# Performance work log

Hardware: AMD Instinct MI355X
Metric: run time of the kernel (lower is better)

## Reference

```python
import jax, jax.numpy as jnp
import numpy as np

B, N, DEG = 128, 512, 8          # graphs, nodes per graph, avg degree
E = B * N * DEG                  # 524288 edges
F_IN, H1, H2, C = 128, 64, 128, 10
RATIO = 0.8
K = int(np.ceil(RATIO * N))      # TopKPooling keeps ceil(0.8*N)=410 nodes per graph


def setup_inputs() -> dict:
    key = jax.random.key(0)
    ks = jax.random.split(key, 10)
    n_nodes = B * N
    x = jax.random.normal(ks[0], (n_nodes, F_IN), dtype=jnp.float32)
    # random intra-graph edges, then offset node ids per graph
    src = jax.random.randint(ks[1], (B, N * DEG), 0, N)
    dst = jax.random.randint(ks[2], (B, N * DEG), 0, N)
    off = (jnp.arange(B) * N)[:, None]
    edge_index = jnp.stack([(src + off).reshape(-1), (dst + off).reshape(-1)]).astype(jnp.int64)
    batch = jnp.repeat(jnp.arange(B), N).astype(jnp.int64)
    s1 = 1.0 / np.sqrt(F_IN)
    s2 = 1.0 / np.sqrt(H1)
    s3 = 1.0 / np.sqrt(H2)
    return {
        "x": x,
        "edge_index": edge_index,
        "batch": batch,
        "W1": jax.random.uniform(ks[3], (F_IN, H1), jnp.float32, -s1, s1),
        "b1": jnp.zeros((H1,), jnp.float32),
        "W2": jax.random.uniform(ks[4], (H1, H2), jnp.float32, -s2, s2),
        "b2": jnp.zeros((H2,), jnp.float32),
        "pool_w": jax.random.uniform(ks[5], (H2,), jnp.float32, -s3, s3),
        "fc_W": jax.random.uniform(ks[6], (H2, C), jnp.float32, -s3, s3),
        "fc_b": jax.random.uniform(ks[7], (C,), jnp.float32, -s3, s3),
    }


def gcn_conv(x, W, b, src, dst, num_nodes):
    # PyG GCNConv: add self-loops, symmetric normalization, scatter-add aggregation
    loop = jnp.arange(num_nodes)
    src = jnp.concatenate([src, loop])
    dst = jnp.concatenate([dst, loop])
    deg = jax.ops.segment_sum(jnp.ones_like(src, dtype=x.dtype), dst, num_segments=num_nodes)
    dis = jnp.where(deg > 0, jax.lax.rsqrt(jnp.maximum(deg, 1.0)), 0.0)
    norm = dis[src] * dis[dst]                       # [E+N]
    h = x @ W                                        # transform first (smaller of the two in conv1)
    out = jax.ops.segment_sum(norm[:, None] * h[src], dst, num_segments=num_nodes)
    return out + b


def reference(x, edge_index, batch, W1, b1, W2, b2, pool_w, fc_W, fc_b):
    num_nodes = x.shape[0]
    src, dst = edge_index[0], edge_index[1]
    x = jax.nn.relu(gcn_conv(x, W1, b1, src, dst, num_nodes))
    x = jax.nn.relu(gcn_conv(x, W2, b2, src, dst, num_nodes))
    # TopKPooling: score = (x . w)/||w||, per-graph top-k on raw score, gate by tanh(score)
    score = (x @ pool_w) / jnp.linalg.norm(pool_w)   # [B*N]
    score_b = score.reshape(B, N)
    top_vals, top_idx = jax.lax.top_k(score_b, K)    # [B, K]
    x_b = x.reshape(B, N, H2)
    x_sel = jnp.take_along_axis(x_b, top_idx[:, :, None], axis=1)   # [B, K, H2]
    x_sel = x_sel * jnp.tanh(top_vals)[:, :, None]
    # global max pool over each (pooled) graph; pooled edge_index is unused downstream
    g = jnp.max(x_sel, axis=1)                        # [B, H2]
    logits = g @ fc_W + fc_b                          # [B, C]
    return jax.nn.log_softmax(logits, axis=1)
```

## Files before the change

kernel.cpp:

```cpp
#include <hip/hip_runtime.h>
#include <hip/hip_bf16.h>


#define BB 128
#define NN 512
#define NODES (BB*NN)
#define EE (BB*NN*8)
#define EDGPG (NN*8)
#define F_IN 128
#define H1 64
#define H2 128
#define NC 10
#define KSEL 410
#define ROWCAP 48

typedef unsigned short u16;
typedef unsigned int   u32;

static __device__ __forceinline__ float lo2f(u32 u){ return __uint_as_float(u << 16); }
static __device__ __forceinline__ float hi2f(u32 u){ return __uint_as_float(u & 0xffff0000u); }
static __device__ __forceinline__ u16 f2b(float f){
    __hip_bfloat16 h = __float2bfloat16(f);
    return *reinterpret_cast<u16*>(&h);
}
static __device__ __forceinline__ u32 packbf(float a, float b){
    return (u32)f2b(a) | ((u32)f2b(b) << 16);
}
static __device__ __forceinline__ void acc8s(float* a, uint4 v, float ds){
    a[0] = fmaf(ds, lo2f(v.x), a[0]); a[1] = fmaf(ds, hi2f(v.x), a[1]);
    a[2] = fmaf(ds, lo2f(v.y), a[2]); a[3] = fmaf(ds, hi2f(v.y), a[3]);
    a[4] = fmaf(ds, lo2f(v.z), a[4]); a[5] = fmaf(ds, hi2f(v.z), a[5]);
    a[6] = fmaf(ds, lo2f(v.w), a[6]); a[7] = fmaf(ds, hi2f(v.w), a[7]);
}
static __device__ __forceinline__ void acc8(float* a, uint4 v){
    a[0] += lo2f(v.x); a[1] += hi2f(v.x);
    a[2] += lo2f(v.y); a[3] += hi2f(v.y);
    a[4] += lo2f(v.z); a[5] += hi2f(v.z);
    a[6] += lo2f(v.w); a[7] += hi2f(v.w);
}
static __device__ __forceinline__ int swz2048(int bid){
    return ((bid & 7) << 8) | (bid >> 3);
}
static __device__ __forceinline__ int swz1024(int bid){
    return ((bid & 7) << 7) | (bid >> 3);
}

static __device__ __forceinline__ bool ei_is_i64(const int* __restrict__ ei){
    return ((ei[1] | ei[3] | ei[5] | ei[7]) == 0);
}
static __device__ __forceinline__ int ld_src(const int* __restrict__ ei, int e, bool w64){
    return w64 ? ei[2*e] : ei[e];
}
static __device__ __forceinline__ int ld_dst(const int* __restrict__ ei, int e, bool w64){
    return w64 ? ei[2*(EE + e)] : ei[EE + e];
}

__global__ __launch_bounds__(512) void k_build(const int* __restrict__ ei,
                                               int* __restrict__ cnt,
                                               int* __restrict__ adj){
    bool w64 = ei_is_i64(ei);
    int t = threadIdx.x;
    int e = (int)blockIdx.x*512 + t;
    int b = e >> 12;
    int d = (ld_dst(ei, e, w64) - b*NN) & (NN - 1);
    int s = ld_src(ei, e, w64) & (NODES - 1);
    int node = b*NN + d;
    int p = atomicAdd(&cnt[node], 1);
    if (p < ROWCAP - 1) adj[node*ROWCAP + 1 + p] = s;
    if (blockIdx.x < BB){
        int sn = (int)blockIdx.x*NN + t;
        adj[sn*ROWCAP] = sn;
    }
}

#define G1NODES 64
#define XPAD 68
__global__ __launch_bounds__(512) void k_gemm1(const float* __restrict__ x,
                                               const float* __restrict__ W1,
                                               u32* __restrict__ h1u){
    __shared__ __align__(16) float Ws[64*H1];
    __shared__ __align__(16) float xs[G1NODES*XPAD];
    int t = threadIdx.x;
    int node0 = (int)blockIdx.x*G1NODES;
    int tc = t & 15, tr = t >> 4;
    int j0 = tc*4, n0 = tr*2;
    float acc[2][4] = {};
    for (int half = 0; half < 2; ++half){
        const float4* Wv = (const float4*)(W1 + half*4096);
        for (int i = t; i < 1024; i += 512)
            *(float4*)&Ws[i*4] = Wv[i];
        for (int i = t; i < 1024; i += 512){
            int node = i >> 4, c = i & 15;
            float4 v = *(const float4*)(x + (size_t)(node0 + node)*F_IN + half*64 + c*4);
            *(float4*)&xs[node*XPAD + c*4] = v;
        }
        __syncthreads();
        #pragma unroll 2
        for (int k = 0; k < 64; k += 4){
            float4 xv0 = *(const float4*)&xs[(n0+0)*XPAD + k];
            float4 xv1 = *(const float4*)&xs[(n0+1)*XPAD + k];
            float xa0[4] = {xv0.x, xv0.y, xv0.z, xv0.w};
            float xa1[4] = {xv1.x, xv1.y, xv1.z, xv1.w};
            #pragma unroll
            for (int kk = 0; kk < 4; ++kk){
                float4 wv = *(const float4*)&Ws[(k+kk)*H1 + j0];
                acc[0][0] += xa0[kk]*wv.x; acc[0][1] += xa0[kk]*wv.y; acc[0][2] += xa0[kk]*wv.z; acc[0][3] += xa0[kk]*wv.w;
                acc[1][0] += xa1[kk]*wv.x; acc[1][1] += xa1[kk]*wv.y; acc[1][2] += xa1[kk]*wv.z; acc[1][3] += xa1[kk]*wv.w;
            }
        }
        __syncthreads();
    }
    #pragma unroll
    for (int i = 0; i < 2; ++i){
        int node = node0 + n0 + i;
        size_t base = (size_t)node*32 + tc*2;
        h1u[base]     = packbf(acc[i][0], acc[i][1]);
        h1u[base + 1] = packbf(acc[i][2], acc[i][3]);
    }
}

__global__ __launch_bounds__(256) void k_agg1(const uint4* __restrict__ h1v,
                                              const int* __restrict__ cnt,
                                              const int* __restrict__ adj,
                                              const float4* __restrict__ b1v,
                                              uint4* __restrict__ a1v){
    __shared__ float disl[NN];
    int t = threadIdx.x;
    int lb = swz2048((int)blockIdx.x);
    int node0 = lb*32;
    int gbase = node0 & ~(NN - 1);
    for (int i = t; i < NN; i += 256){
        int c = cnt[gbase + i]; if (c > ROWCAP-1) c = ROWCAP-1;
        disl[i] = rsqrtf((float)(c + 1));
    }
    __syncthreads();
    int node = node0 + (t >> 3);
    int fl = t & 7;
    int rs = node*ROWCAP;
    int c = cnt[node]; if (c > ROWCAP-1) c = ROWCAP-1;
    int pe = rs + c + 1;
    float a0[8] = {}, a1r[8] = {}, a2r[8] = {}, a3r[8] = {};
    int p = rs;
    for (; p + 4 <= pe; p += 4){
        int s0 = adj[p], s1 = adj[p+1], s2 = adj[p+2], s3 = adj[p+3];
        float d0 = disl[s0 & (NN-1)], d1 = disl[s1 & (NN-1)];
        float d2 = disl[s2 & (NN-1)], d3 = disl[s3 & (NN-1)];
        uint4 v0 = h1v[s0*8 + fl];
        uint4 v1 = h1v[s1*8 + fl];
        uint4 v2 = h1v[s2*8 + fl];
        uint4 v3 = h1v[s3*8 + fl];
        acc8s(a0, v0, d0); acc8s(a1r, v1, d1); acc8s(a2r, v2, d2); acc8s(a3r, v3, d3);
    }
    for (; p < pe; ++p){
        int s = adj[p];
        acc8s(a0, h1v[s*8 + fl], disl[s & (NN-1)]);
    }
    float r[8];
    #pragma unroll
    for (int j = 0; j < 8; ++j) r[j] = (a0[j] + a1r[j]) + (a2r[j] + a3r[j]);
    float dn = disl[node & (NN-1)];
    float4 bA = b1v[2*fl], bB = b1v[2*fl+1];
    float w0 = dn*r[0] + bA.x; w0 = w0 > 0.f ? w0 : 0.f;
    float w1 = dn*r[1] + bA.y; w1 = w1 > 0.f ? w1 : 0.f;
    float w2 = dn*r[2] + bA.z; w2 = w2 > 0.f ? w2 : 0.f;
    float w3 = dn*r[3] + bA.w; w3 = w3 > 0.f ? w3 : 0.f;
    float w4 = dn*r[4] + bB.x; w4 = w4 > 0.f ? w4 : 0.f;
    float w5 = dn*r[5] + bB.y; w5 = w5 > 0.f ? w5 : 0.f;
    float w6 = dn*r[6] + bB.z; w6 = w6 > 0.f ? w6 : 0.f;
    float w7 = dn*r[7] + bB.w; w7 = w7 > 0.f ? w7 : 0.f;
    a1v[node*8 + fl] = make_uint4(packbf(dn*w0, dn*w1), packbf(dn*w2, dn*w3),
                                  packbf(dn*w4, dn*w5), packbf(dn*w6, dn*w7));
}

#define G2NODES 64
#define APAD 68
__global__ __launch_bounds__(256) void k_gemm2s(const uint4* __restrict__ a1v,
                                                const int* __restrict__ cnt,
                                                const int* __restrict__ adj,
                                                const float* __restrict__ W2,
                                                const float* __restrict__ b2,
                                                const float* __restrict__ pw,
                                                u32* __restrict__ a2u,
                                                float* __restrict__ score){
    __shared__ __align__(16) float Ws[32*H2];
    __shared__ __align__(16) float as[G2NODES*APAD];
    __shared__ float pws[H2];
    int t = threadIdx.x;
    int lb = swz1024((int)blockIdx.x);
    int node0 = lb*G2NODES;
    if (t < H2) pws[t] = pw[t];
    {
        int fl = t & 7, ng = t >> 3;
        for (int pass = 0; pass < 2; ++pass){
            int nl = ng + pass*32;
            int node = node0 + nl;
            int rs = node*ROWCAP;
            int c = cnt[node]; if (c > ROWCAP-1) c = ROWCAP-1;
            int pe = rs + c + 1;
            float a0[8] = {}, a1r[8] = {}, a2r[8] = {}, a3r[8] = {};
            int p = rs;
            for (; p + 4 <= pe; p += 4){
                int s0 = adj[p], s1 = adj[p+1], s2 = adj[p+2], s3 = adj[p+3];
                uint4 v0 = a1v[s0*8 + fl];
                uint4 v1 = a1v[s1*8 + fl];
                uint4 v2 = a1v[s2*8 + fl];
                uint4 v3 = a1v[s3*8 + fl];
                acc8(a0, v0); acc8(a1r, v1); acc8(a2r, v2); acc8(a3r, v3);
            }
            for (; p < pe; ++p){
                uint4 v = a1v[adj[p]*8 + fl];
                acc8(a0, v);
            }
            float dn = rsqrtf((float)(c + 1));
            float* dst = &as[nl*APAD + 8*fl];
            float r0 = dn*((a0[0] + a1r[0]) + (a2r[0] + a3r[0]));
            float r1 = dn*((a0[1] + a1r[1]) + (a2r[1] + a3r[1]));
            float r2 = dn*((a0[2] + a1r[2]) + (a2r[2] + a3r[2]));
            float r3 = dn*((a0[3] + a1r[3]) + (a2r[3] + a3r[3]));
            float r4 = dn*((a0[4] + a1r[4]) + (a2r[4] + a3r[4]));
            float r5 = dn*((a0[5] + a1r[5]) + (a2r[5] + a3r[5]));
            float r6 = dn*((a0[6] + a1r[6]) + (a2r[6] + a3r[6]));
            float r7 = dn*((a0[7] + a1r[7]) + (a2r[7] + a3r[7]));
            *(float4*)&dst[0] = make_float4(r0, r1, r2, r3);
            *(float4*)&dst[4] = make_float4(r4, r5, r6, r7);
        }
    }
    int tc = t & 15, tr = t >> 4;
    int j0 = tc*8;
    float acc[4][8] = {};
    for (int half = 0; half < 2; ++half){
        const float4* Wv = (const float4*)(W2 + half*4096);
        for (int i = t; i < 1024; i += 256)
            *(float4*)&Ws[i*4] = Wv[i];
        __syncthreads();
        int kb = half*32;
        #pragma unroll 2
        for (int k = 0; k < 32; k += 4){
            float4 xv0 = *(const float4*)&as[(tr +  0)*APAD + kb + k];
            float4 xv1 = *(const float4*)&as[(tr + 16)*APAD + kb + k];
            float4 xv2 = *(const float4*)&as[(tr + 32)*APAD + kb + k];
            float4 xv3 = *(const float4*)&as[(tr + 48)*APAD + kb + k];
            float xa0[4] = {xv0.x, xv0.y, xv0.z, xv0.w};
            float xa1[4] = {xv1.x, xv1.y, xv1.z, xv1.w};
            float xa2[4] = {xv2.x, xv2.y, xv2.z, xv2.w};
            float xa3[4] = {xv3.x, xv3.y, xv3.z, xv3.w};
            #pragma unroll
            for (int kk = 0; kk < 4; ++kk){
                float4 wa = *(const float4*)&Ws[(k+kk)*H2 + j0];
                float4 wb = *(const float4*)&Ws[(k+kk)*H2 + j0 + 4];
                acc[0][0] += xa0[kk]*wa.x; acc[0][1] += xa0[kk]*wa.y; acc[0][2] += xa0[kk]*wa.z; acc[0][3] += xa0[kk]*wa.w;
                acc[0][4] += xa0[kk]*wb.x; acc[0][5] += xa0[kk]*wb.y; acc[0][6] += xa0[kk]*wb.z; acc[0][7] += xa0[kk]*wb.w;
                acc[1][0] += xa1[kk]*wa.x; acc[1][1] += xa1[kk]*wa.y; acc[1][2] += xa1[kk]*wa.z; acc[1][3] += xa1[kk]*wa.w;
                acc[1][4] += xa1[kk]*wb.x; acc[1][5] += xa1[kk]*wb.y; acc[1][6] += xa1[kk]*wb.z; acc[1][7] += xa1[kk]*wb.w;
                acc[2][0] += xa2[kk]*wa.x; acc[2][1] += xa2[kk]*wa.y; acc[2][2] += xa2[kk]*wa.z; acc[2][3] += xa2[kk]*wa.w;
                acc[2][4] += xa2[kk]*wb.x; acc[2][5] += xa2[kk]*wb.y; acc[2][6] += xa2[kk]*wb.z; acc[2][7] += xa2[kk]*wb.w;
                acc[3][0] += xa3[kk]*wa.x; acc[3][1] += xa3[kk]*wa.y; acc[3][2] += xa3[kk]*wa.z; acc[3][3] += xa3[kk]*wa.w;
                acc[3][4] += xa3[kk]*wb.x; acc[3][5] += xa3[kk]*wb.y; acc[3][6] += xa3[kk]*wb.z; acc[3][7] += xa3[kk]*wb.w;
            }
        }
        __syncthreads();
    }
    float p0 = pws[j0],   p1 = pws[j0+1], p2 = pws[j0+2], p3 = pws[j0+3];
    float p4 = pws[j0+4], p5 = pws[j0+5], p6 = pws[j0+6], p7 = pws[j0+7];
    float bj[8];
    #pragma unroll
    for (int c2 = 0; c2 < 8; ++c2) bj[c2] = b2[j0 + c2];
    #pragma unroll
    for (int i = 0; i < 4; ++i){
        int node = node0 + tr + 16*i;
        float v0 = acc[i][0] + bj[0]; v0 = v0 > 0.f ? v0 : 0.f;
        float v1 = acc[i][1] + bj[1]; v1 = v1 > 0.f ? v1 : 0.f;
        float v2 = acc[i][2] + bj[2]; v2 = v2 > 0.f ? v2 : 0.f;
        float v3 = acc[i][3] + bj[3]; v3 = v3 > 0.f ? v3 : 0.f;
        float v4 = acc[i][4] + bj[4]; v4 = v4 > 0.f ? v4 : 0.f;
        float v5 = acc[i][5] + bj[5]; v5 = v5 > 0.f ? v5 : 0.f;
        float v6 = acc[i][6] + bj[6]; v6 = v6 > 0.f ? v6 : 0.f;
        float v7 = acc[i][7] + bj[7]; v7 = v7 > 0.f ? v7 : 0.f;
        *(uint4*)&a2u[(size_t)node*64 + tc*4] =
            make_uint4(packbf(v0, v1), packbf(v2, v3), packbf(v4, v5), packbf(v6, v7));
        float sp = v0*p0 + v1*p1 + v2*p2 + v3*p3 + v4*p4 + v5*p5 + v6*p6 + v7*p7;
        sp += __shfl_xor(sp, 8, 16);
        sp += __shfl_xor(sp, 4, 16);
        sp += __shfl_xor(sp, 2, 16);
        sp += __shfl_xor(sp, 1, 16);
        if (tc == 0) score[node] = sp;
    }
}

__global__ __launch_bounds__(512) void k_pool(const u32* __restrict__ a2u,
                                              const float* __restrict__ score,
                                              const float* __restrict__ pw,
                                              const float* __restrict__ fcW,
                                              const float* __restrict__ fcb,
                                              float* __restrict__ out){
    __shared__ float so[NN];
    __shared__ float ss[NN];
    __shared__ float th[NN];
    __shared__ float pm[32*H2];
    __shared__ float gl[H2];
    __shared__ float fws[H2*NC];
    __shared__ float lg[NC];
    __shared__ float red[3];
    int b = blockIdx.x, t = threadIdx.x;
    for (int i = t; i < H2*NC; i += 512) fws[i] = fcW[i];
    if (t < H2){ float v = pw[t]; gl[t] = v*v; }
    __syncthreads();
    if (t == 0){
        float s = 0.f;
        for (int i = 0; i < H2; ++i) s += gl[i];
        red[2] = rsqrtf(s);
    }
    __syncthreads();
    float pwinv = red[2];
    float sc = score[b*NN + t];
    so[t] = sc; th[t] = tanhf(sc*pwinv);
    float v = sc;
    for (int k = 2; k <= NN; k <<= 1){
        for (int j = k >> 1; j > 0; j >>= 1){
            bool desc  = ((t & k) == 0);
            bool lower = ((t & j) == 0);
            bool wantmax = (desc == lower);
            float c;
            if (j >= 64){
                ss[t] = v; __syncthreads();
                c = ss[t ^ j];
                __syncthreads();
            } else {
                c = __shfl_xor(v, j, 64);
            }
            v = wantmax ? fmaxf(v, c) : fminf(v, c);
        }
    }
    ss[t] = v;
    __syncthreads();
    float thresh = ss[KSEL-1];
    float mask_t = (so[t] >= thresh) ? 0.f : -INFINITY;
    __syncthreads();
    so[t] = mask_t;
    __syncthreads();
    int tc = t & 15, q = t >> 4;
    const uint4* ap = (const uint4*)(a2u + (size_t)b*NN*64);
    float m0 = -INFINITY, m1 = -INFINITY, m2 = -INFINITY, m3 = -INFINITY;
    float m4 = -INFINITY, m5 = -INFINITY, m6 = -INFINITY, m7 = -INFINITY;
    int nb = q*16;
    #pragma unroll 4
    for (int n = nb; n < nb + 16; ++n){
        uint4 vv = ap[(size_t)n*16 + tc];
        float thn = th[n], son = so[n];
        m0 = fmaxf(m0, lo2f(vv.x)*thn + son);
        m1 = fmaxf(m1, hi2f(vv.x)*thn + son);
        m2 = fmaxf(m2, lo2f(vv.y)*thn + son);
        m3 = fmaxf(m3, hi2f(vv.y)*thn + son);
        m4 = fmaxf(m4, lo2f(vv.z)*thn + son);
        m5 = fmaxf(m5, hi2f(vv.z)*thn + son);
        m6 = fmaxf(m6, lo2f(vv.w)*thn + son);
        m7 = fmaxf(m7, hi2f(vv.w)*thn + son);
    }
    float* pmr = &pm[q*H2 + 8*tc];
    pmr[0] = m0; pmr[1] = m1; pmr[2] = m2; pmr[3] = m3;
    pmr[4] = m4; pmr[5] = m5; pmr[6] = m6; pmr[7] = m7;
    __syncthreads();
    if (t < H2){
        float g = pm[t];
        #pragma unroll
        for (int qq = 1; qq < 32; ++qq) g = fmaxf(g, pm[qq*H2 + t]);
        gl[t] = g;
    }
    __syncthreads();
    if (t < NC){
        float acc = fcb[t];
        for (int k2 = 0; k2 < H2; ++k2) acc += gl[k2]*fws[k2*NC + t];
        lg[t] = acc;
    }
    __syncthreads();
    if (t == 0){
        float mx = lg[0];
        for (int i = 1; i < NC; ++i) mx = fmaxf(mx, lg[i]);
        float s = 0.f;
        for (int i = 0; i < NC; ++i) s += expf(lg[i] - mx);
        red[0] = mx; red[1] = logf(s);
    }
    __syncthreads();
    if (t < NC) out[b*NC + t] = lg[t] - red[0] - red[1];
}

extern "C" void kernel_launch(void* const* d_in, const int* in_sizes, int n_in,
                              void* d_out, int out_size, void* d_ws, size_t ws_size,
                              hipStream_t stream) {
    const float* x   = (const float*)d_in[0];
    const int*   ei  = (const int*)d_in[1];
    const float* W1  = (const float*)d_in[3];
    const float* b1  = (const float*)d_in[4];
    const float* W2  = (const float*)d_in[5];
    const float* b2  = (const float*)d_in[6];
    const float* pw  = (const float*)d_in[7];
    const float* fcW = (const float*)d_in[8];
    const float* fcb = (const float*)d_in[9];

    char* ws = (char*)d_ws;
    int*   cnt   = (int*)(ws + 4096);
    float* score = (float*)(ws + 524288);
    int*   adj   = (int*)(ws + 4194304);
    u32*   h1u   = (u32*)(ws + 16777216);
    u32*   a1u   = (u32*)(ws + 25165824);
    u32*   a2u   = (u32*)(ws + 33554432);

    hipMemsetAsync(cnt, 0, NODES*sizeof(int), stream);
    k_build<<<EE/512, 512, 0, stream>>>(ei, cnt, adj);
    k_gemm1<<<NODES/G1NODES, 512, 0, stream>>>(x, W1, h1u);
    k_agg1<<<NODES/32, 256, 0, stream>>>((const uint4*)h1u, cnt, adj,
                                         (const float4*)b1, (uint4*)a1u);
    k_gemm2s<<<NODES/G2NODES, 256, 0, stream>>>((const uint4*)a1u, cnt, adj,
                                                W2, b2, pw, a2u, score);
    k_pool<<<BB, 512, 0, stream>>>(a2u, score, pw, fcW, fcb, (float*)d_out);
}
```

Measured before the change: 181.5 us.

## Fuse adjacency build into gemm1, split layer-2 aggregation from its GEMM

Measured after the change: 180.9 us. No clear change (-0.3%).

```diff
diff --git a/kernel.cpp b/kernel.cpp
--- a/kernel.cpp
+++ b/kernel.cpp
@@ -55,33 +55,36 @@
     return w64 ? ei[2*(EE + e)] : ei[EE + e];
 }
 
-__global__ __launch_bounds__(512) void k_build(const int* __restrict__ ei,
-                                               int* __restrict__ cnt,
-                                               int* __restrict__ adj){
+#define G1NODES 64
+#define XPAD 68
+__global__ __launch_bounds__(512) void k_prep_gemm1(const int* __restrict__ ei,
+                                                    const float* __restrict__ x,
+                                                    const float* __restrict__ W1,
+                                                    int* __restrict__ cnt,
+                                                    int* __restrict__ adj,
+                                                    u32* __restrict__ h1u){
+    __shared__ __align__(16) float Ws[64*H1];
+    __shared__ __align__(16) float xs[G1NODES*XPAD];
     bool w64 = ei_is_i64(ei);
     int t = threadIdx.x;
-    int e = (int)blockIdx.x*512 + t;
-    int b = e >> 12;
-    int d = (ld_dst(ei, e, w64) - b*NN) & (NN - 1);
-    int s = ld_src(ei, e, w64) & (NODES - 1);
-    int node = b*NN + d;
-    int p = atomicAdd(&cnt[node], 1);
-    if (p < ROWCAP - 1) adj[node*ROWCAP + 1 + p] = s;
-    if (blockIdx.x < BB){
-        int sn = (int)blockIdx.x*NN + t;
-        adj[sn*ROWCAP] = sn;
-    }
-}
-
-#define G1NODES 64
-#define XPAD 68
-__global__ __launch_bounds__(512) void k_gemm1(const float* __restrict__ x,
-                                               const float* __restrict__ W1,
-                                               u32* __restrict__ h1u){
-    __shared__ __align__(16) float Ws[64*H1];
-    __shared__ __align__(16) float xs[G1NODES*XPAD];
-    int t = threadIdx.x;
-    int node0 = (int)blockIdx.x*G1NODES;
+    int gb = (int)blockIdx.x;
+    int b  = gb >> 3;
+    int sub = gb & 7;
+    int node0 = b*NN + sub*G1NODES;
+
+    {
+        int e = b*EDGPG + sub*512 + t;
+        int d = (ld_dst(ei, e, w64) - b*NN) & (NN - 1);
+        int s = ld_src(ei, e, w64) & (NODES - 1);
+        int node = b*NN + d;
+        int p = atomicAdd(&cnt[node], 1);
+        if (p < ROWCAP - 1) adj[node*ROWCAP + 1 + p] = s;
+    }
+    if (t < G1NODES){
+        int node = node0 + t;
+        adj[node*ROWCAP] = node;
+    }
+
     int tc = t & 15, tr = t >> 4;
     int j0 = tc*4, n0 = tr*2;
     float acc[2][4] = {};
@@ -172,16 +175,49 @@
                                   packbf(dn*w4, dn*w5), packbf(dn*w6, dn*w7));
 }
 
+__global__ __launch_bounds__(256) void k_agg2(const uint4* __restrict__ a1v,
+                                              const int* __restrict__ cnt,
+                                              const int* __restrict__ adj,
+                                              float4* __restrict__ aggf){
+    int t = threadIdx.x;
+    int lb = swz2048((int)blockIdx.x);
+    int node = lb*32 + (t >> 3);
+    int fl = t & 7;
+    int rs = node*ROWCAP;
+    int c = cnt[node]; if (c > ROWCAP-1) c = ROWCAP-1;
+    int pe = rs + c + 1;
+    float a0[8] = {}, b0[8] = {}, c0[8] = {}, d0[8] = {};
+    int p = rs;
+    for (; p + 4 <= pe; p += 4){
+        int s0 = adj[p], s1 = adj[p+1], s2 = adj[p+2], s3 = adj[p+3];
+        uint4 v0 = a1v[s0*8 + fl];
+        uint4 v1 = a1v[s1*8 + fl];
+        uint4 v2 = a1v[s2*8 + fl];
+        uint4 v3 = a1v[s3*8 + fl];
+        acc8(a0, v0); acc8(b0, v1); acc8(c0, v2); acc8(d0, v3);
+    }
+    for (; p < pe; ++p) acc8(a0, a1v[adj[p]*8 + fl]);
+    float dn = rsqrtf((float)(c + 1));
+    float r0 = dn*((a0[0]+b0[0]) + (c0[0]+d0[0]));
+    float r1 = dn*((a0[1]+b0[1]) + (c0[1]+d0[1]));
+    float r2 = dn*((a0[2]+b0[2]) + (c0[2]+d0[2]));
+    float r3 = dn*((a0[3]+b0[3]) + (c0[3]+d0[3]));
+    float r4 = dn*((a0[4]+b0[4]) + (c0[4]+d0[4]));
+    float r5 = dn*((a0[5]+b0[5]) + (c0[5]+d0[5]));
+    float r6 = dn*((a0[6]+b0[6]) + (c0[6]+d0[6]));
+    float r7 = dn*((a0[7]+b0[7]) + (c0[7]+d0[7]));
+    aggf[(size_t)node*16 + fl*2]     = make_float4(r0, r1, r2, r3);
+    aggf[(size_t)node*16 + fl*2 + 1] = make_float4(r4, r5, r6, r7);
+}
+
 #define G2NODES 64
 #define APAD 68
-__global__ __launch_bounds__(256) void k_gemm2s(const uint4* __restrict__ a1v,
-                                                const int* __restrict__ cnt,
-                                                const int* __restrict__ adj,
-                                                const float* __restrict__ W2,
-                                                const float* __restrict__ b2,
-                                                const float* __restrict__ pw,
-                                                u32* __restrict__ a2u,
-                                                float* __restrict__ score){
+__global__ __launch_bounds__(512) void k_gemm2sc(const float4* __restrict__ aggf,
+                                                 const float* __restrict__ W2,
+                                                 const float* __restrict__ b2,
+                                                 const float* __restrict__ pw,
+                                                 u32* __restrict__ a2u,
+                                                 float* __restrict__ score){
     __shared__ __align__(16) float Ws[32*H2];
     __shared__ __align__(16) float as[G2NODES*APAD];
     __shared__ float pws[H2];
@@ -189,73 +225,39 @@
     int lb = swz1024((int)blockIdx.x);
     int node0 = lb*G2NODES;
     if (t < H2) pws[t] = pw[t];
-    {
-        int fl = t & 7, ng = t >> 3;
-        for (int pass = 0; pass < 2; ++pass){
-            int nl = ng + pass*32;
-            int node = node0 + nl;
-            int rs = node*ROWCAP;
-            int c = cnt[node]; if (c > ROWCAP-1) c = ROWCAP-1;
-            int pe = rs + c + 1;
-            float a0[8] = {}, a1r[8] = {}, a2r[8] = {}, a3r[8] = {};
-            int p = rs;
-            for (; p + 4 <= pe; p += 4){
-                int s0 = adj[p], s1 = adj[p+1], s2 = adj[p+2], s3 = adj[p+3];
-                uint4 v0 = a1v[s0*8 + fl];
-                uint4 v1 = a1v[s1*8 + fl];
-                uint4 v2 = a1v[s2*8 + fl];
-                uint4 v3 = a1v[s3*8 + fl];
-                acc8(a0, v0); acc8(a1r, v1); acc8(a2r, v2); acc8(a3r, v3);
-            }
-            for (; p < pe; ++p){
-                uint4 v = a1v[adj[p]*8 + fl];
-                acc8(a0, v);
-            }
-            float dn = rsqrtf((float)(c + 1));
-            float* dst = &as[nl*APAD + 8*fl];
-            float r0 = dn*((a0[0] + a1r[0]) + (a2r[0] + a3r[0]));
-            float r1 = dn*((a0[1] + a1r[1]) + (a2r[1] + a3r[1]));
-            float r2 = dn*((a0[2] + a1r[2]) + (a2r[2] + a3r[2]));
-            float r3 = dn*((a0[3] + a1r[3]) + (a2r[3] + a3r[3]));
-            float r4 = dn*((a0[4] + a1r[4]) + (a2r[4] + a3r[4]));
-            float r5 = dn*((a0[5] + a1r[5]) + (a2r[5] + a3r[5]));
-            float r6 = dn*((a0[6] + a1r[6]) + (a2r[6] + a3r[6]));
-            float r7 = dn*((a0[7] + a1r[7]) + (a2r[7] + a3r[7]));
-            *(float4*)&dst[0] = make_float4(r0, r1, r2, r3);
-            *(float4*)&dst[4] = make_float4(r4, r5, r6, r7);
-        }
+    #pragma unroll
+    for (int kf = 0; kf < 2; ++kf){
+        int idx = t + kf*512;
+        int row = idx >> 4, c = idx & 15;
+        *(float4*)&as[row*APAD + c*4] = aggf[(size_t)(node0 + row)*16 + c];
     }
     int tc = t & 15, tr = t >> 4;
-    int j0 = tc*8;
-    float acc[4][8] = {};
+    int j0 = tc*8, n0 = tr*2;
+    float acc[2][8] = {};
     for (int half = 0; half < 2; ++half){
         const float4* Wv = (const float4*)(W2 + half*4096);
-        for (int i = t; i < 1024; i += 256)
+        for (int i = t; i < 1024; i += 512)
             *(float4*)&Ws[i*4] = Wv[i];
         __syncthreads();
         int kb = half*32;
         #pragma unroll 2
         for (int k = 0; k < 32; k += 4){
-            float4 xv0 = *(const float4*)&as[(tr +  0)*APAD + kb + k];
-            float4 xv1 = *(const float4*)&as[(tr + 16)*APAD + kb + k];
-            float4 xv2 = *(const float4*)&as[(tr + 32)*APAD + kb + k];
-            float4 xv3 = *(const float4*)&as[(tr + 48)*APAD + kb + k];
+            float4 xv0 = *(const float4*)&as[(n0+0)*APAD + kb + k];
+            float4 xv1 = *(const float4*)&as[(n0+1)*APAD + kb + k];
             float xa0[4] = {xv0.x, xv0.y, xv0.z, xv0.w};
             float xa1[4] = {xv1.x, xv1.y, xv1.z, xv1.w};
-            float xa2[4] = {xv2.x, xv2.y, xv2.z, xv2.w};
-            float xa3[4] = {xv3.x, xv3.y, xv3.z, xv3.w};
             #pragma unroll
             for (int kk = 0; kk < 4; ++kk){
                 float4 wa = *(const float4*)&Ws[(k+kk)*H2 + j0];
                 float4 wb = *(const float4*)&Ws[(k+kk)*H2 + j0 + 4];
-                acc[0][0] += xa0[kk]*wa.x; acc[0][1] += xa0[kk]*wa.y; acc[0][2] += xa0[kk]*wa.z; acc[0][3] += xa0[kk]*wa.w;
-                acc[0][4] += xa0[kk]*wb.x; acc[0][5] += xa0[kk]*wb.y; acc[0][6] += xa0[kk]*wb.z; acc[0][7] += xa0[kk]*wb.w;
-                acc[1][0] += xa1[kk]*wa.x; acc[1][1] += xa1[kk]*wa.y; acc[1][2] += xa1[kk]*wa.z; acc[1][3] += xa1[kk]*wa.w;
-                acc[1][4] += xa1[kk]*wb.x; acc[1][5] += xa1[kk]*wb.y; acc[1][6] += xa1[kk]*wb.z; acc[1][7] += xa1[kk]*wb.w;
-                acc[2][0] += xa2[kk]*wa.x; acc[2][1] += xa2[kk]*wa.y; acc[2][2] += xa2[kk]*wa.z; acc[2][3] += xa2[kk]*wa.w;
-                acc[2][4] += xa2[kk]*wb.x; acc[2][5] += xa2[kk]*wb.y; acc[2][6] += xa2[kk]*wb.z; acc[2][7] += xa2[kk]*wb.w;
-                acc[3][0] += xa3[kk]*wa.x; acc[3][1] += xa3[kk]*wa.y; acc[3][2] += xa3[kk]*wa.z; acc[3][3] += xa3[kk]*wa.w;
-                acc[3][4] += xa3[kk]*wb.x; acc[3][5] += xa3[kk]*wb.y; acc[3][6] += xa3[kk]*wb.z; acc[3][7] += xa3[kk]*wb.w;
+                acc[0][0] += xa0[kk]*wa.x; acc[0][1] += xa0[kk]*wa.y;
+                acc[0][2] += xa0[kk]*wa.z; acc[0][3] += xa0[kk]*wa.w;
+                acc[0][4] += xa0[kk]*wb.x; acc[0][5] += xa0[kk]*wb.y;
+                acc[0][6] += xa0[kk]*wb.z; acc[0][7] += xa0[kk]*wb.w;
+                acc[1][0] += xa1[kk]*wa.x; acc[1][1] += xa1[kk]*wa.y;
+                acc[1][2] += xa1[kk]*wa.z; acc[1][3] += xa1[kk]*wa.w;
+                acc[1][4] += xa1[kk]*wb.x; acc[1][5] += xa1[kk]*wb.y;
+                acc[1][6] += xa1[kk]*wb.z; acc[1][7] += xa1[kk]*wb.w;
             }
         }
         __syncthreads();
@@ -266,8 +268,8 @@
     #pragma unroll
     for (int c2 = 0; c2 < 8; ++c2) bj[c2] = b2[j0 + c2];
     #pragma unroll
-    for (int i = 0; i < 4; ++i){
-        int node = node0 + tr + 16*i;
+    for (int i = 0; i < 2; ++i){
+        int node = node0 + n0 + i;
         float v0 = acc[i][0] + bj[0]; v0 = v0 > 0.f ? v0 : 0.f;
         float v1 = acc[i][1] + bj[1]; v1 = v1 > 0.f ? v1 : 0.f;
         float v2 = acc[i][2] + bj[2]; v2 = v2 > 0.f ? v2 : 0.f;
@@ -301,9 +303,10 @@
     __shared__ float fws[H2*NC];
     __shared__ float lg[NC];
     __shared__ float red[3];
-    int b = blockIdx.x, t = threadIdx.x;
+    int bid = blockIdx.x, t = threadIdx.x;
+    int b = ((bid & 7) << 4) | (bid >> 3);
     for (int i = t; i < H2*NC; i += 512) fws[i] = fcW[i];
-    if (t < H2){ float v = pw[t]; gl[t] = v*v; }
+    if (t < H2){ float v2 = pw[t]; gl[t] = v2*v2; }
     __syncthreads();
     if (t == 0){
         float s = 0.f;
@@ -403,14 +406,16 @@
     int*   adj   = (int*)(ws + 4194304);
     u32*   h1u   = (u32*)(ws + 16777216);
     u32*   a1u   = (u32*)(ws + 25165824);
-    u32*   a2u   = (u32*)(ws + 33554432);
+    float* aggf  = (float*)(ws + 33554432);
+    u32*   a2u   = (u32*)(ws + 50331648);
 
     hipMemsetAsync(cnt, 0, NODES*sizeof(int), stream);
-    k_build<<<EE/512, 512, 0, stream>>>(ei, cnt, adj);
-    k_gemm1<<<NODES/G1NODES, 512, 0, stream>>>(x, W1, h1u);
+    k_prep_gemm1<<<NODES/G1NODES, 512, 0, stream>>>(ei, x, W1, cnt, adj, h1u);
     k_agg1<<<NODES/32, 256, 0, stream>>>((const uint4*)h1u, cnt, adj,
                                          (const float4*)b1, (uint4*)a1u);
-    k_gemm2s<<<NODES/G2NODES, 256, 0, stream>>>((const uint4*)a1u, cnt, adj,
-                                                W2, b2, pw, a2u, score);
+    k_agg2<<<NODES/32, 256, 0, stream>>>((const uint4*)a1u, cnt, adj,
+                                         (float4*)aggf);
+    k_gemm2sc<<<NODES/G2NODES, 512, 0, stream>>>((const float4*)aggf, W2, b2, pw,
+                                                 a2u, score);
     k_pool<<<BB, 512, 0, stream>>>(a2u, score, pw, fcW, fcb, (float*)d_out);
 }
```
